# Optimization experiments

Measured on AMD Instinct MI355X. Metric: run time of the kernel, lower is better.

The kernel has to match this reference:

```python
import jax, jax.numpy as jnp
import numpy as np

K_NEIGHBORS = 9  # top_k, dilation=1 for both blocks


def causal_conv1d(x, w, b, dilation):
    # x: [B, Cin, W]; w: [Cout, Cin, K]. Conv1d(padding=p both sides) + Chomp(p) == left-pad only.
    pad = (w.shape[-1] - 1) * dilation
    y = jax.lax.conv_general_dilated(
        x, w, window_strides=(1,), padding=[(pad, 0)], rhs_dilation=(dilation,),
        dimension_numbers=('NCH', 'OIH', 'NCH'))
    return y + b[None, :, None]


def knn_indices(xt, k):
    # xt: [B, N, C] node features. F.normalize(p=2) along channels, then top-k by -||xi-xj||^2.
    xn = xt / jnp.maximum(jnp.linalg.norm(xt, axis=-1, keepdims=True), 1e-12)
    sq = jnp.sum(xn * xn, axis=-1)  # [B, N]
    neg_dist = 2.0 * jnp.einsum('bnc,bmc->bnm', xn, xn) - sq[:, :, None] - sq[:, None, :]
    _, idx = jax.lax.top_k(neg_dist, k)  # [B, N, k]
    return idx


def edge_conv_block(xt, w, b, gamma, beta):
    # xt: [B, N, C]. EdgeConv: max_k gelu(BN(Conv1x1(cat[x_i, x_j - x_i]))) with residual.
    idx = knn_indices(xt, K_NEIGHBORS)
    # gather neighbors: x_j[b,n,k,c] = xt[b, idx[b,n,k], c]
    x_j = jnp.take_along_axis(xt[:, :, None, :], idx[..., None], axis=1)  # [B,N,k,C]
    x_i = xt[:, :, None, :]
    feat = jnp.concatenate([jnp.broadcast_to(x_i, x_j.shape), x_j - x_i], axis=-1)  # [B,N,k,2C]
    h = jnp.einsum('bnkc,oc->bnko', feat, w) + b  # 1x1 conv over 2C -> C
    h = h * gamma + beta  # eval BatchNorm2d (fresh running stats) == affine
    h = jax.nn.gelu(h, approximate=False)
    return xt + jnp.max(h, axis=2)  # residual, [B,N,C]


def ffn_block(xt, w1, b1, g1, be1, w2, b2, g2, be2):
    h = jnp.einsum('bnc,oc->bno', xt, w1) + b1
    h = jax.nn.gelu(h * g1 + be1, approximate=False)
    h = jnp.einsum('bnc,oc->bno', h, w2) + b2
    return h * g2 + be2  # note: this FFN has no residual in the source


def setup_inputs() -> dict:
    key = jax.random.key(0)
    ks = jax.random.split(key, 12)
    B, M, W = 16, 100, 2048
    s = 0.05
    inp = {
        'ts': jax.random.normal(ks[0], (B, M, W), jnp.float32),
        'conv1_w': jax.random.normal(ks[1], (64, M, 3), jnp.float32) * s,
        'conv1_b': jax.random.normal(ks[2], (64,), jnp.float32) * s,
        'conv2_w': jax.random.normal(ks[3], (128, 64, 3), jnp.float32) * s,
        'conv2_b': jax.random.normal(ks[4], (128,), jnp.float32) * s,
        'gconv_w': jax.random.normal(ks[5], (2, 128, 256), jnp.float32) * s,
        'gconv_b': jax.random.normal(ks[6], (2, 128), jnp.float32) * s,
        'gconv_gamma': jnp.ones((2, 128), jnp.float32),
        'gconv_beta': jnp.zeros((2, 128), jnp.float32),
        'ffn1_w': jax.random.normal(ks[7], (2, 128, 128), jnp.float32) * s,
        'ffn1_b': jax.random.normal(ks[8], (2, 128), jnp.float32) * s,
        'ffn1_gamma': jnp.ones((2, 128), jnp.float32),
        'ffn1_beta': jnp.zeros((2, 128), jnp.float32),
        'ffn2_w': jax.random.normal(ks[9], (2, 128, 128), jnp.float32) * s,
        'ffn2_b': jax.random.normal(ks[10], (2, 128), jnp.float32) * s,
        'ffn2_gamma': jnp.ones((2, 128), jnp.float32),
        'ffn2_beta': jnp.zeros((2, 128), jnp.float32),
    }
    return inp


def reference(ts, conv1_w, conv1_b, conv2_w, conv2_b,
              gconv_w, gconv_b, gconv_gamma, gconv_beta,
              ffn1_w, ffn1_b, ffn1_gamma, ffn1_beta,
              ffn2_w, ffn2_b, ffn2_gamma, ffn2_beta):
    # InnerEncoder: two causal dilated Conv1d + ReLU (dropout=0, eval)
    h = jax.nn.relu(causal_conv1d(ts, conv1_w, conv1_b, dilation=1))
    h = jax.nn.relu(causal_conv1d(h, conv2_w, conv2_b, dilation=2))  # [B,128,W]
    xt = h.transpose(0, 2, 1)  # [B, N=W, C=128] nodes
    for blk in range(2):
        xt = edge_conv_block(xt, gconv_w[blk], gconv_b[blk], gconv_gamma[blk], gconv_beta[blk])
        xt = ffn_block(xt, ffn1_w[blk], ffn1_b[blk], ffn1_gamma[blk], ffn1_beta[blk],
                       ffn2_w[blk], ffn2_b[blk], ffn2_gamma[blk], ffn2_beta[blk])
    return xt  # [B, W, 128] == encoderdata.permute(0,2,1)
```

## Files before the change

kernel.cpp:

```cpp
#include <hip/hip_runtime.h>
#include <hip/hip_bf16.h>

#define DEV_INLINE __device__ __forceinline__

typedef short s16x8 __attribute__((ext_vector_type(8)));
typedef float f32x4 __attribute__((ext_vector_type(4)));

DEV_INLINE float gelu_exact(float x) {
    return 0.5f * x * (1.0f + erff(x * 0.70710678118654752440f));
}
DEV_INLINE double gelu64(double x) {
    return 0.5 * x * (1.0 + erf(x * 0.70710678118654752440));
}
DEV_INLINE unsigned short f2bf_rne(float f) {
    unsigned u = __float_as_uint(f);
    unsigned r = u + 0x7FFFu + ((u >> 16) & 1u);
    return (unsigned short)(r >> 16);
}
DEV_INLINE float bf2f(unsigned short h) { return __uint_as_float(((unsigned)h) << 16); }

DEV_INLINE void gload_lds16(const void* g, void* l) {
    __builtin_amdgcn_global_load_lds(
        (const __attribute__((address_space(1))) unsigned int*)g,
        (__attribute__((address_space(3))) unsigned int*)l, 16, 0, 0);
}

DEV_INLINE unsigned med3u32(unsigned a, unsigned b, unsigned c) {
    unsigned d;
    asm("v_med3_u32 %0, %1, %2, %3" : "=v"(d) : "v"(a), "v"(b), "v"(c));
    return d;
}

__global__ __launch_bounds__(256) void conv1_kernel64(
    const float* __restrict__ x, const float* __restrict__ w,
    const float* __restrict__ bias, double* __restrict__ y)
{
    const int b = blockIdx.y;
    const int t0 = blockIdx.x * 32;
    __shared__ double xs[100][34];
    for (int e = threadIdx.x; e < 100 * 34; e += 256) {
        int i = e / 34, u = e - i * 34;
        int t = t0 - 2 + u;
        xs[i][u] = (t >= 0) ? (double)x[(b * 100 + i) * 2048 + t] : 0.0;
    }
    __syncthreads();
    const int o = threadIdx.x & 63;
    const int ts = (threadIdx.x >> 6) * 8;
    double acc[8];
    double bv = (double)bias[o];
#pragma unroll
    for (int j = 0; j < 8; ++j) acc[j] = bv;
    const float* wo = w + o * 300;
    for (int i = 0; i < 100; ++i) {
        double w0 = (double)wo[i * 3 + 0], w1 = (double)wo[i * 3 + 1], w2 = (double)wo[i * 3 + 2];
#pragma unroll
        for (int j = 0; j < 8; ++j) {
            acc[j] = fma(w0, xs[i][ts + j],
                     fma(w1, xs[i][ts + j + 1],
                     fma(w2, xs[i][ts + j + 2], acc[j])));
        }
    }
#pragma unroll
    for (int j = 0; j < 8; ++j)
        y[(b * 64 + o) * 2048 + t0 + ts + j] = fmax(acc[j], 0.0);
}

__global__ __launch_bounds__(256) void conv2_kernel64(
    const double* __restrict__ x, const float* __restrict__ w,
    const float* __restrict__ bias, double* __restrict__ xt)
{
    const int b = blockIdx.y;
    const int t0 = blockIdx.x * 32;
    __shared__ double xs[64][36];
    for (int e = threadIdx.x; e < 64 * 36; e += 256) {
        int i = e / 36, u = e - i * 36;
        int t = t0 - 4 + u;
        xs[i][u] = (t >= 0) ? x[(b * 64 + i) * 2048 + t] : 0.0;
    }
    __syncthreads();
    const int o = threadIdx.x & 127;
    const int ts = (threadIdx.x >> 7) * 16;
    double acc[16];
    double bv = (double)bias[o];
#pragma unroll
    for (int j = 0; j < 16; ++j) acc[j] = bv;
    const float* wo = w + o * 192;
    for (int i = 0; i < 64; ++i) {
        double w0 = (double)wo[i * 3 + 0], w1 = (double)wo[i * 3 + 1], w2 = (double)wo[i * 3 + 2];
#pragma unroll
        for (int j = 0; j < 16; ++j) {
            acc[j] = fma(w0, xs[i][ts + j],
                     fma(w1, xs[i][ts + j + 2],
                     fma(w2, xs[i][ts + j + 4], acc[j])));
        }
    }
#pragma unroll
    for (int j = 0; j < 16; ++j)
        xt[(size_t)(b * 2048 + t0 + ts + j) * 128 + o] = fmax(acc[j], 0.0);
}

__global__ __launch_bounds__(256) void norm_planes_kernel(
    const double* __restrict__ xt64, unsigned short* __restrict__ XH,
    unsigned short* __restrict__ XM, double* __restrict__ XN64,
    double* __restrict__ SQ64)
{
    const int row = blockIdx.x * 4 + (threadIdx.x >> 6);
    const int lane = threadIdx.x & 63;
    double v0 = xt64[(size_t)row * 128 + lane * 2];
    double v1 = xt64[(size_t)row * 128 + lane * 2 + 1];
    double s = v0 * v0 + v1 * v1;
#pragma unroll
    for (int off = 32; off > 0; off >>= 1) s += __shfl_xor(s, off);
    double inv = 1.0 / fmax(sqrt(s), 1e-12);
    double n0 = v0 * inv, n1 = v1 * inv;
    XN64[(size_t)row * 128 + lane * 2]     = n0;
    XN64[(size_t)row * 128 + lane * 2 + 1] = n1;
    double q = n0 * n0 + n1 * n1;
#pragma unroll
    for (int off = 32; off > 0; off >>= 1) q += __shfl_xor(q, off);
    if (lane == 0) SQ64[row] = q;
    float x0 = (float)n0, x1 = (float)n1;
    unsigned short h0 = f2bf_rne(x0), h1 = f2bf_rne(x1);
    unsigned short m0 = f2bf_rne(x0 - bf2f(h0)), m1 = f2bf_rne(x1 - bf2f(h1));
    ushort2 hv; hv.x = h0; hv.y = h1;
    ushort2 mv; mv.x = m0; mv.y = m1;
    *(ushort2*)(XH + (size_t)row * 128 + lane * 2) = hv;
    *(ushort2*)(XM + (size_t)row * 128 + lane * 2) = mv;
}

#define INS9(cc) do { \
    unsigned c_ = (cc); \
    unsigned n0_ = (k0 > c_) ? k0 : c_; \
    unsigned n1_ = med3u32(k0, k1, c_); \
    unsigned n2_ = med3u32(k1, k2, c_); \
    unsigned n3_ = med3u32(k2, k3, c_); \
    unsigned n4_ = med3u32(k3, k4, c_); \
    unsigned n5_ = med3u32(k4, k5, c_); \
    unsigned n6_ = med3u32(k5, k6, c_); \
    unsigned n7_ = med3u32(k6, k7, c_); \
    unsigned n8_ = med3u32(k7, k8, c_); \
    k0 = n0_; k1 = n1_; k2 = n2_; k3 = n3_; k4 = n4_; \
    k5 = n5_; k6 = n6_; k7 = n7_; k8 = n8_; \
} while (0)

__global__ __launch_bounds__(512, 2) void knn_mfma9_kernel(
    const unsigned short* __restrict__ XH, const unsigned short* __restrict__ XM,
    int* __restrict__ cand_out)
{
    __shared__ __align__(16) unsigned char smem[65536];

    const int tid = threadIdx.x, wave = tid >> 6, lane = tid & 63;
    const int bid = blockIdx.x;
    const int j = bid >> 3;
    const int b = (bid & 7) * 2 + (j >> 5);
    const int ntile = (j & 31) >> 1;
    const int mhalf = j & 1;
    const int n0 = ntile * 128;
    const int mstart = mhalf * 1024;
    const unsigned short* Hb = XH + (size_t)b * 2048 * 128;
    const unsigned short* Mb = XM + (size_t)b * 2048 * 128;

    s16x8 aH[4], aM[4];
    {
        int arow = n0 + wave * 16 + (lane & 15);
        const unsigned short* hrow = Hb + (size_t)arow * 128;
        const unsigned short* mrow = Mb + (size_t)arow * 128;
        int cb = (lane >> 4) * 8;
#pragma unroll
        for (int s = 0; s < 4; ++s) {
            aH[s] = *(const s16x8*)(hrow + s * 32 + cb);
            aM[s] = *(const s16x8*)(mrow + s * 32 + cb);
        }
    }

    const unsigned short* Pb = (wave >> 2) ? Mb : Hb;
    const unsigned short* gsrc0; const unsigned short* gsrc1;
    const unsigned short* gsrc2; const unsigned short* gsrc3;
    {
        int r0 = (wave & 3) * 16 + 0 + (lane >> 4), c0 = (lane & 15) ^ (r0 & 7);
        int r1 = (wave & 3) * 16 + 4 + (lane >> 4), c1 = (lane & 15) ^ (r1 & 7);
        int r2 = (wave & 3) * 16 + 8 + (lane >> 4), c2 = (lane & 15) ^ (r2 & 7);
        int r3 = (wave & 3) * 16 + 12 + (lane >> 4), c3 = (lane & 15) ^ (r3 & 7);
        gsrc0 = Pb + (size_t)(mstart + r0) * 128 + c0 * 8;
        gsrc1 = Pb + (size_t)(mstart + r1) * 128 + c1 * 8;
        gsrc2 = Pb + (size_t)(mstart + r2) * 128 + c2 * 8;
        gsrc3 = Pb + (size_t)(mstart + r3) * 128 + c3 * 8;
    }
    const unsigned ldsbase = (wave * 4) * 1024;

    unsigned k0 = 0, k1 = 0, k2 = 0, k3 = 0, k4 = 0, k5 = 0, k6 = 0, k7 = 0, k8 = 0;

    gload_lds16(gsrc0, smem + ldsbase);
    gload_lds16(gsrc1, smem + ldsbase + 1024);
    gload_lds16(gsrc2, smem + ldsbase + 2048);
    gload_lds16(gsrc3, smem + ldsbase + 3072);
    __syncthreads();

    int cur = 0;
    for (int t = 0; t < 16; ++t) {
        if (t < 15) {
            size_t go = (size_t)(t + 1) * 64 * 128;
            unsigned lb = (cur ^ 1) * 32768 + ldsbase;
            gload_lds16(gsrc0 + go, smem + lb);
            gload_lds16(gsrc1 + go, smem + lb + 1024);
            gload_lds16(gsrc2 + go, smem + lb + 2048);
            gload_lds16(gsrc3 + go, smem + lb + 3072);
        }
        const unsigned char* B0 = smem + cur * 32768;
        const unsigned char* B1 = B0 + 16384;
#pragma unroll
        for (int ct = 0; ct < 4; ++ct) {
            f32x4 accA; accA[0] = 0.f; accA[1] = 0.f; accA[2] = 0.f; accA[3] = 0.f;
            f32x4 accB; accB[0] = 0.f; accB[1] = 0.f; accB[2] = 0.f; accB[3] = 0.f;
            int r = ct * 16 + (lane & 15);
#pragma unroll
            for (int s = 0; s < 4; ++s) {
                int off = r * 256 + (((s * 64) + ((lane >> 4) * 16)) ^ ((r & 7) << 4));
                s16x8 bH = *(const s16x8*)(B0 + off);
                s16x8 bM = *(const s16x8*)(B1 + off);
                accA = __builtin_amdgcn_mfma_f32_16x16x32_bf16(bH, aH[s], accA, 0, 0, 0);
                accB = __builtin_amdgcn_mfma_f32_16x16x32_bf16(bM, aH[s], accB, 0, 0, 0);
                accB = __builtin_amdgcn_mfma_f32_16x16x32_bf16(bH, aM[s], accB, 0, 0, 0);
            }
            const unsigned Lb = (unsigned)(255 - (t * 16 + ct * 4));
            unsigned key0 = (__float_as_uint(accA[0] + accB[0] + 2.0f) & 0xFFFFFF00u) | (Lb - 0u);
            unsigned key1 = (__float_as_uint(accA[1] + accB[1] + 2.0f) & 0xFFFFFF00u) | (Lb - 1u);
            unsigned key2 = (__float_as_uint(accA[2] + accB[2] + 2.0f) & 0xFFFFFF00u) | (Lb - 2u);
            unsigned key3 = (__float_as_uint(accA[3] + accB[3] + 2.0f) & 0xFFFFFF00u) | (Lb - 3u);
            INS9(key0);
            INS9(key1);
            INS9(key2);
            INS9(key3);
        }
        __syncthreads();
        cur ^= 1;
    }

    const int g = lane >> 4;
    const int row = b * 2048 + n0 + wave * 16 + (lane & 15);
#pragma unroll
    for (int pass = 0; pass < 16; ++pass) {
        unsigned mykey = k0;
        int L = 255 - (int)(mykey & 0xFFu);
        int mym = mstart + (L >> 4) * 64 + ((L >> 2) & 3) * 16 + g * 4 + (L & 3);
        unsigned bkey = mykey; int bm = mym;
        unsigned ok = (unsigned)__shfl_xor((int)bkey, 16); int om = __shfl_xor(bm, 16);
        bool tk = (ok > bkey) || (ok == bkey && om < bm);
        bkey = tk ? ok : bkey; bm = tk ? om : bm;
        ok = (unsigned)__shfl_xor((int)bkey, 32); om = __shfl_xor(bm, 32);
        tk = (ok > bkey) || (ok == bkey && om < bm);
        bkey = tk ? ok : bkey; bm = tk ? om : bm;
        if (mym == bm) {
            k0 = k1; k1 = k2; k2 = k3; k3 = k4; k4 = k5; k5 = k6; k6 = k7; k7 = k8; k8 = 0;
        }
        if (g == (pass & 3)) cand_out[(size_t)row * 32 + mhalf * 16 + pass] = bm;
    }
}

__global__ __launch_bounds__(256, 4) void rescore5_kernel(
    const double* __restrict__ XN64, const double* __restrict__ SQ64,
    const int* __restrict__ cand, int* __restrict__ idx_out)
{
    const int wid = threadIdx.x >> 6, lane = threadIdx.x & 63;
    const int wb = (blockIdx.x & 7) * 1024 + (blockIdx.x >> 3);
    const int n = wb * 4 + wid;
    const int b = n >> 11;
    const int g = lane >> 4, e = lane & 15;
    const double* Xb = XN64 + (size_t)(b * 2048) * 128;
    const double* SQb = SQ64 + (size_t)b * 2048;

    double2 xq[4];
    const double* xqp = XN64 + (size_t)n * 128;
#pragma unroll
    for (int it = 0; it < 4; ++it)
        xq[it] = *(const double2*)(xqp + it * 32 + e * 2);

    int mi[8];
    double s[8];
#pragma unroll
    for (int bb = 0; bb < 8; ++bb) {
        int m = cand[(size_t)n * 32 + bb * 4 + g];
        mi[bb] = m;
        const double* xm = Xb + (size_t)m * 128;
        double a0 = 0.0, a1 = 0.0;
#pragma unroll
        for (int it = 0; it < 4; ++it) {
            double2 v = *(const double2*)(xm + it * 32 + e * 2);
            a0 = fma(xq[it].x, v.x, a0);
            a1 = fma(xq[it].y, v.y, a1);
        }
        s[bb] = a0 + a1;
    }
#pragma unroll
    for (int bb = 0; bb < 8; ++bb) {
        double d = s[bb];
        d += __shfl_xor(d, 1);
        d += __shfl_xor(d, 2);
        d += __shfl_xor(d, 4);
        d += __shfl_xor(d, 8);
        s[bb] = 2.0 * d - SQb[mi[bb]];
    }
    double mys = s[0]; int mym = mi[0];
#pragma unroll
    for (int q = 1; q < 8; ++q) {
        bool p = (e == q);
        mys = p ? s[q] : mys;
        mym = p ? mi[q] : mym;
    }
    int cnt = 0;
#pragma unroll
    for (int bb = 0; bb < 8; ++bb) {
        cnt += ((s[bb] > mys) || (s[bb] == mys && mi[bb] < mym)) ? 1 : 0;
        double a16 = __shfl_xor(s[bb], 16); int m16 = __shfl_xor(mi[bb], 16);
        cnt += ((a16 > mys) || (a16 == mys && m16 < mym)) ? 1 : 0;
        double a32 = __shfl_xor(s[bb], 32); int m32 = __shfl_xor(mi[bb], 32);
        cnt += ((a32 > mys) || (a32 == mys && m32 < mym)) ? 1 : 0;
        double a48 = __shfl_xor(a16, 32);  int m48 = __shfl_xor(m16, 32);
        cnt += ((a48 > mys) || (a48 == mys && m48 < mym)) ? 1 : 0;
    }
    if (e < 8 && cnt < 9)
        idx_out[(size_t)n * 9 + cnt] = mym;
}

template<int MODE>
__global__ __launch_bounds__(256, 4) void gemm64t_kernel(
    const double* __restrict__ A, const float* __restrict__ W,
    const float* __restrict__ bias, const float* __restrict__ gamma,
    const float* __restrict__ beta, double* __restrict__ out,
    float* __restrict__ out32)
{
    __shared__ double As[64][34];
    __shared__ double Ws[64][34];
    const int bx = (blockIdx.x & 7) * (gridDim.x >> 3) + (blockIdx.x >> 3);
    const int m0 = bx * 64;
    const int j0 = blockIdx.y * 64;
    const int ri = threadIdx.x >> 4, ci = threadIdx.x & 15;
    double acc[4][4];
#pragma unroll
    for (int u = 0; u < 4; ++u)
#pragma unroll
        for (int v = 0; v < 4; ++v) acc[u][v] = 0.0;

    for (int k0 = 0; k0 < 128; k0 += 32) {
        __syncthreads();
        for (int e = threadIdx.x; e < 64 * 16; e += 256) {
            int r = e >> 4, c2 = (e & 15) * 2;
            *(double2*)&As[r][c2] = *(const double2*)(A + (size_t)(m0 + r) * 128 + k0 + c2);
            int jw = j0 + r;
            float2 wv;
            if (MODE == 0) {
                wv = (jw < 128) ? *(const float2*)(W + jw * 256 + k0 + c2)
                                : *(const float2*)(W + (jw - 128) * 256 + 128 + k0 + c2);
            } else {
                wv = *(const float2*)(W + jw * 128 + k0 + c2);
            }
            double2 wd; wd.x = (double)wv.x; wd.y = (double)wv.y;
            *(double2*)&Ws[r][c2] = wd;
        }
        __syncthreads();
        for (int c = 0; c < 32; c += 2) {
            double a0[4], a1[4], w0[4], w1[4];
#pragma unroll
            for (int u = 0; u < 4; ++u) { a0[u] = As[ri + 16 * u][c]; a1[u] = As[ri + 16 * u][c + 1]; }
#pragma unroll
            for (int v = 0; v < 4; ++v) { w0[v] = Ws[ci + 16 * v][c]; w1[v] = Ws[ci + 16 * v][c + 1]; }
#pragma unroll
            for (int u = 0; u < 4; ++u)
#pragma unroll
                for (int v = 0; v < 4; ++v)
                    acc[u][v] = fma(a1[u], w1[v], fma(a0[u], w0[v], acc[u][v]));
        }
    }
#pragma unroll
    for (int u = 0; u < 4; ++u) {
        int row = m0 + ri + 16 * u;
#pragma unroll
        for (int v = 0; v < 4; ++v) {
            int jl = ci + 16 * v;
            double val = acc[u][v];
            if (MODE == 0) {
                out[(size_t)row * 256 + j0 + jl] = val;
            } else {
                int jg = j0 + jl;
                double z = (val + (double)bias[jg]) * (double)gamma[jg] + (double)beta[jg];
                if (MODE == 1) {
                    out[(size_t)row * 128 + jg] = gelu64(z);
                } else {
                    out[(size_t)row * 128 + jg] = z;
                    out32[(size_t)row * 128 + jg] = (float)z;
                }
            }
        }
    }
}

__global__ __launch_bounds__(256) void combine64_kernel(
    double* __restrict__ xt, const double* __restrict__ G,
    const int* __restrict__ idx, const float* __restrict__ bias,
    const float* __restrict__ gamma, const float* __restrict__ beta)
{
    const int wb = (blockIdx.x & 7) * 2048 + (blockIdx.x >> 3);
    const int row = wb * 2 + (threadIdx.x >> 7);
    const int o = threadIdx.x & 127;
    const int b = row >> 11;
    const double* Gb = G + (size_t)(b * 2048) * 256;
    const int* id9 = idx + (size_t)row * 9;
    double g1  = G[(size_t)row * 256 + o];
    double g2i = G[(size_t)row * 256 + 128 + o];
    double base = g1 + (double)bias[o] - g2i;
    double gm = (double)gamma[o], bt = (double)beta[o];
    double mx = -1.0e300;
#pragma unroll
    for (int k = 0; k < 9; ++k) {
        int jn = id9[k];
        double h = base + Gb[(size_t)jn * 256 + 128 + o];
        double z = h * gm + bt;
        mx = fmax(mx, gelu64(z));
    }
    xt[(size_t)row * 128 + o] += mx;
}

template<int MODE>
__global__ __launch_bounds__(256) void gemm128t_kernel(
    const float* __restrict__ A, const float* __restrict__ W,
    const float* __restrict__ bias, const float* __restrict__ gamma,
    const float* __restrict__ beta, float* __restrict__ out)
{
    __shared__ float Al[128][132];
    __shared__ float Wl[128][132];
    const int bx = (blockIdx.x & 7) * (gridDim.x >> 3) + (blockIdx.x >> 3);
    const int m0 = bx * 128;
    const int j0 = blockIdx.y * 128;
    for (int e = threadIdx.x; e < 128 * 32; e += 256) {
        int r = e >> 5, q = e & 31;
        *(float4*)&Al[r][q * 4] = *(const float4*)(A + (size_t)(m0 + r) * 128 + q * 4);
    }
    for (int e = threadIdx.x; e < 128 * 32; e += 256) {
        int jj = e >> 5, q = e & 31;
        int c = q * 4;
        const float* src;
        if (MODE == 0) {
            int jw = j0 + jj;
            src = (jw < 128) ? (W + jw * 256 + c) : (W + (jw - 128) * 256 + 128 + c);
        } else {
            src = W + jj * 128 + c;
        }
        *(float4*)&Wl[jj][c] = *(const float4*)src;
    }
    __syncthreads();
    const int ri = threadIdx.x >> 4, ci = threadIdx.x & 15;
    float acc[8][8];
#pragma unroll
    for (int u = 0; u < 8; ++u)
#pragma unroll
        for (int v = 0; v < 8; ++v) acc[u][v] = 0.0f;
    for (int c = 0; c < 128; c += 4) {
        float4 a4[8];
#pragma unroll
        for (int u = 0; u < 8; ++u) a4[u] = *(const float4*)&Al[ri + 16 * u][c];
#pragma unroll
        for (int v = 0; v < 8; ++v) {
            float4 w4 = *(const float4*)&Wl[ci + 16 * v][c];
#pragma unroll
            for (int u = 0; u < 8; ++u) {
                acc[u][v] = fmaf(a4[u].x, w4.x, fmaf(a4[u].y, w4.y,
                            fmaf(a4[u].z, w4.z, fmaf(a4[u].w, w4.w, acc[u][v]))));
            }
        }
    }
#pragma unroll
    for (int u = 0; u < 8; ++u) {
        int row = m0 + ri + 16 * u;
#pragma unroll
        for (int v = 0; v < 8; ++v) {
            int jn = ci + 16 * v;
            float val = acc[u][v];
            if (MODE == 0) {
                out[(size_t)row * 256 + j0 + jn] = val;
            } else if (MODE == 1) {
                float z = (val + bias[jn]) * gamma[jn] + beta[jn];
                out[(size_t)row * 128 + jn] = gelu_exact(z);
            } else {
                float z = (val + bias[jn]) * gamma[jn] + beta[jn];
                out[(size_t)row * 128 + jn] = z;
            }
        }
    }
}

__global__ __launch_bounds__(256) void combine_kernel(
    const float* __restrict__ xt, const float* __restrict__ G,
    const int* __restrict__ idx, const float* __restrict__ bias,
    const float* __restrict__ gamma, const float* __restrict__ beta,
    float* __restrict__ xt2)
{
    const int wb = (blockIdx.x & 7) * 2048 + (blockIdx.x >> 3);
    const int row = wb * 2 + (threadIdx.x >> 7);
    const int o = threadIdx.x & 127;
    const int b = row >> 11;
    const float* Gb = G + (size_t)(b * 2048) * 256;
    const int* id9 = idx + (size_t)row * 9;
    float g1  = G[(size_t)row * 256 + o];
    float g2i = G[(size_t)row * 256 + 128 + o];
    float base = g1 + bias[o] - g2i;
    float gm = gamma[o], bt = beta[o];
    float mx = -3.4e38f;
#pragma unroll
    for (int k = 0; k < 9; ++k) {
        int jn = id9[k];
        float h = base + Gb[(size_t)jn * 256 + 128 + o];
        float z = h * gm + bt;
        mx = fmaxf(mx, gelu_exact(z));
    }
    xt2[(size_t)row * 128 + o] = xt[(size_t)row * 128 + o] + mx;
}

extern "C" void kernel_launch(void* const* d_in, const int* in_sizes, int n_in,
                              void* d_out, int out_size, void* d_ws, size_t ws_size,
                              hipStream_t stream)
{
    const float* ts       = (const float*)d_in[0];
    const float* conv1_w  = (const float*)d_in[1];
    const float* conv1_b  = (const float*)d_in[2];
    const float* conv2_w  = (const float*)d_in[3];
    const float* conv2_b  = (const float*)d_in[4];
    const float* gconv_w  = (const float*)d_in[5];
    const float* gconv_b  = (const float*)d_in[6];
    const float* gconv_g  = (const float*)d_in[7];
    const float* gconv_be = (const float*)d_in[8];
    const float* ffn1_w   = (const float*)d_in[9];
    const float* ffn1_b   = (const float*)d_in[10];
    const float* ffn1_g   = (const float*)d_in[11];
    const float* ffn1_be  = (const float*)d_in[12];
    const float* ffn2_w   = (const float*)d_in[13];
    const float* ffn2_b   = (const float*)d_in[14];
    const float* ffn2_g   = (const float*)d_in[15];
    const float* ffn2_be  = (const float*)d_in[16];
    (void)in_sizes; (void)n_in; (void)out_size; (void)ws_size;

    char* base = (char*)d_ws;
    double*         XT64   = (double*)(base + 0);
    double*         H1_64  = (double*)(base + 33554432);
    unsigned short* XH     = (unsigned short*)(base + 33554432);
    unsigned short* XM     = (unsigned short*)(base + 41943040);
    int*            CAND   = (int*)   (base + 50331648);
    double*         XN64_1 = (double*)(base + 54525952);
    double*         SQ64_1 = (double*)(base + 88080384);
    double*         G64    = (double*)(base + 33554432);
    double*         H64    = (double*)(base + 33554432);
    float*          XT32P  = (float*) (base + 67108864);
    int*            IDX    = (int*)   (base + 100663296);
    float*          G32    = (float*) (base + 33554432);
    float*          H32    = (float*) (base + 33554432);
    double*         XN64_2 = XT64;
    double*         SQ64_2 = SQ64_1;

    float* fout = (float*)d_out;

    conv1_kernel64<<<dim3(64, 16), 256, 0, stream>>>(ts, conv1_w, conv1_b, H1_64);
    conv2_kernel64<<<dim3(64, 16), 256, 0, stream>>>(H1_64, conv2_w, conv2_b, XT64);

    norm_planes_kernel<<<8192, 256, 0, stream>>>(XT64, XH, XM, XN64_1, SQ64_1);
    knn_mfma9_kernel<<<512, 512, 0, stream>>>(XH, XM, CAND);
    rescore5_kernel<<<8192, 256, 0, stream>>>(XN64_1, SQ64_1, CAND, IDX);
    gemm64t_kernel<0><<<dim3(512, 4), 256, 0, stream>>>(
        XT64, gconv_w, nullptr, nullptr, nullptr, G64, nullptr);
    combine64_kernel<<<16384, 256, 0, stream>>>(
        XT64, G64, IDX, gconv_b, gconv_g, gconv_be);
    gemm64t_kernel<1><<<dim3(512, 2), 256, 0, stream>>>(
        XT64, ffn1_w, ffn1_b, ffn1_g, ffn1_be, H64, nullptr);
    gemm64t_kernel<2><<<dim3(512, 2), 256, 0, stream>>>(
        H64, ffn2_w, ffn2_b, ffn2_g, ffn2_be, XT64, XT32P);

    norm_planes_kernel<<<8192, 256, 0, stream>>>(XT64, XH, XM, XN64_2, SQ64_2);
    knn_mfma9_kernel<<<512, 512, 0, stream>>>(XH, XM, CAND);
    rescore5_kernel<<<8192, 256, 0, stream>>>(XN64_2, SQ64_2, CAND, IDX);
    gemm128t_kernel<0><<<dim3(256, 2), 256, 0, stream>>>(
        XT32P, gconv_w + 32768, nullptr, nullptr, nullptr, G32);
    combine_kernel<<<16384, 256, 0, stream>>>(
        XT32P, G32, IDX, gconv_b + 128, gconv_g + 128, gconv_be + 128, XT32P);
    gemm128t_kernel<1><<<dim3(256, 1), 256, 0, stream>>>(
        XT32P, ffn1_w + 16384, ffn1_b + 128, ffn1_g + 128, ffn1_be + 128, H32);
    gemm128t_kernel<2><<<dim3(256, 1), 256, 0, stream>>>(
        H32, ffn2_w + 16384, ffn2_b + 128, ffn2_g + 128, ffn2_be + 128, fout);
}
```

Baseline: 702.4 us.

## Evaluate GELU only at neighbor min/max and retile fp32 GEMMs with K-chunking

In both combine kernels, the max over nine neighbors of gelu(affine(base+g2)) is replaced by tracking only the min and max of g2 and evaluating GELU at those two points. This relies on GELU composed with an affine map being quasi-convex, so its maximum over an interval lies at an endpoint, and it cuts nine erf evaluations to two. The fp32 GEMM moves from 128x128 tiles with full-K shared memory (about 135KB) to 64-row tiles with 32-wide K chunks and a bounds hint of 4 blocks per SM. This raises occupancy and doubles the grid, at the cost of extra barriers per chunk.

```diff
diff --git a/kernel.cpp b/kernel.cpp
--- a/kernel.cpp
+++ b/kernel.cpp
@@ -409,67 +409,75 @@
     double g2i = G[(size_t)row * 256 + 128 + o];
     double base = g1 + (double)bias[o] - g2i;
     double gm = (double)gamma[o], bt = (double)beta[o];
-    double mx = -1.0e300;
+    double g2mx = -1.0e300, g2mn = 1.0e300;
 #pragma unroll
     for (int k = 0; k < 9; ++k) {
         int jn = id9[k];
-        double h = base + Gb[(size_t)jn * 256 + 128 + o];
-        double z = h * gm + bt;
-        mx = fmax(mx, gelu64(z));
-    }
+        double g2 = Gb[(size_t)jn * 256 + 128 + o];
+        g2mx = fmax(g2mx, g2);
+        g2mn = fmin(g2mn, g2);
+    }
+    double h1 = base + g2mx;
+    double h2 = base + g2mn;
+    double z1 = h1 * gm + bt;
+    double z2 = h2 * gm + bt;
+    double mx = fmax(gelu64(z1), gelu64(z2));
     xt[(size_t)row * 128 + o] += mx;
 }
 
 template<int MODE>
-__global__ __launch_bounds__(256) void gemm128t_kernel(
+__global__ __launch_bounds__(256, 4) void gemm32f_kernel(
     const float* __restrict__ A, const float* __restrict__ W,
     const float* __restrict__ bias, const float* __restrict__ gamma,
     const float* __restrict__ beta, float* __restrict__ out)
 {
-    __shared__ float Al[128][132];
-    __shared__ float Wl[128][132];
+    __shared__ float As[64][36];
+    __shared__ float Ws[128][36];
     const int bx = (blockIdx.x & 7) * (gridDim.x >> 3) + (blockIdx.x >> 3);
-    const int m0 = bx * 128;
+    const int m0 = bx * 64;
     const int j0 = blockIdx.y * 128;
-    for (int e = threadIdx.x; e < 128 * 32; e += 256) {
-        int r = e >> 5, q = e & 31;
-        *(float4*)&Al[r][q * 4] = *(const float4*)(A + (size_t)(m0 + r) * 128 + q * 4);
-    }
-    for (int e = threadIdx.x; e < 128 * 32; e += 256) {
-        int jj = e >> 5, q = e & 31;
-        int c = q * 4;
-        const float* src;
-        if (MODE == 0) {
-            int jw = j0 + jj;
-            src = (jw < 128) ? (W + jw * 256 + c) : (W + (jw - 128) * 256 + 128 + c);
-        } else {
-            src = W + jj * 128 + c;
-        }
-        *(float4*)&Wl[jj][c] = *(const float4*)src;
-    }
-    __syncthreads();
     const int ri = threadIdx.x >> 4, ci = threadIdx.x & 15;
-    float acc[8][8];
-#pragma unroll
-    for (int u = 0; u < 8; ++u)
+    float acc[4][8];
+#pragma unroll
+    for (int u = 0; u < 4; ++u)
 #pragma unroll
         for (int v = 0; v < 8; ++v) acc[u][v] = 0.0f;
-    for (int c = 0; c < 128; c += 4) {
-        float4 a4[8];
-#pragma unroll
-        for (int u = 0; u < 8; ++u) a4[u] = *(const float4*)&Al[ri + 16 * u][c];
-#pragma unroll
-        for (int v = 0; v < 8; ++v) {
-            float4 w4 = *(const float4*)&Wl[ci + 16 * v][c];
-#pragma unroll
-            for (int u = 0; u < 8; ++u) {
-                acc[u][v] = fmaf(a4[u].x, w4.x, fmaf(a4[u].y, w4.y,
-                            fmaf(a4[u].z, w4.z, fmaf(a4[u].w, w4.w, acc[u][v]))));
+
+    for (int k0 = 0; k0 < 128; k0 += 32) {
+        __syncthreads();
+        for (int e = threadIdx.x; e < 64 * 8; e += 256) {
+            int r = e >> 3, q = (e & 7) * 4;
+            *(float4*)&As[r][q] = *(const float4*)(A + (size_t)(m0 + r) * 128 + k0 + q);
+        }
+        for (int e = threadIdx.x; e < 128 * 8; e += 256) {
+            int r = e >> 3, q = (e & 7) * 4;
+            const float* src;
+            if (MODE == 0) {
+                int jw = j0 + r;
+                src = (jw < 128) ? (W + jw * 256 + k0 + q) : (W + (jw - 128) * 256 + 128 + k0 + q);
+            } else {
+                src = W + r * 128 + k0 + q;
             }
-        }
-    }
-#pragma unroll
-    for (int u = 0; u < 8; ++u) {
+            *(float4*)&Ws[r][q] = *(const float4*)src;
+        }
+        __syncthreads();
+        for (int c = 0; c < 32; c += 4) {
+            float4 a4[4];
+#pragma unroll
+            for (int u = 0; u < 4; ++u) a4[u] = *(const float4*)&As[ri + 16 * u][c];
+#pragma unroll
+            for (int v = 0; v < 8; ++v) {
+                float4 w4 = *(const float4*)&Ws[ci + 16 * v][c];
+#pragma unroll
+                for (int u = 0; u < 4; ++u) {
+                    acc[u][v] = fmaf(a4[u].x, w4.x, fmaf(a4[u].y, w4.y,
+                                fmaf(a4[u].z, w4.z, fmaf(a4[u].w, w4.w, acc[u][v]))));
+                }
+            }
+        }
+    }
+#pragma unroll
+    for (int u = 0; u < 4; ++u) {
         int row = m0 + ri + 16 * u;
 #pragma unroll
         for (int v = 0; v < 8; ++v) {
@@ -504,14 +512,17 @@
     float g2i = G[(size_t)row * 256 + 128 + o];
     float base = g1 + bias[o] - g2i;
     float gm = gamma[o], bt = beta[o];
-    float mx = -3.4e38f;
+    float g2mx = -3.4e38f, g2mn = 3.4e38f;
 #pragma unroll
     for (int k = 0; k < 9; ++k) {
         int jn = id9[k];
-        float h = base + Gb[(size_t)jn * 256 + 128 + o];
-        float z = h * gm + bt;
-        mx = fmaxf(mx, gelu_exact(z));
-    }
+        float g2 = Gb[(size_t)jn * 256 + 128 + o];
+        g2mx = fmaxf(g2mx, g2);
+        g2mn = fminf(g2mn, g2);
+    }
+    float z1 = (base + g2mx) * gm + bt;
+    float z2 = (base + g2mn) * gm + bt;
+    float mx = fmaxf(gelu_exact(z1), gelu_exact(z2));
     xt2[(size_t)row * 128 + o] = xt[(size_t)row * 128 + o] + mx;
 }
 
@@ -575,12 +586,12 @@
     norm_planes_kernel<<<8192, 256, 0, stream>>>(XT64, XH, XM, XN64_2, SQ64_2);
     knn_mfma9_kernel<<<512, 512, 0, stream>>>(XH, XM, CAND);
     rescore5_kernel<<<8192, 256, 0, stream>>>(XN64_2, SQ64_2, CAND, IDX);
-    gemm128t_kernel<0><<<dim3(256, 2), 256, 0, stream>>>(
+    gemm32f_kernel<0><<<dim3(512, 2), 256, 0, stream>>>(
         XT32P, gconv_w + 32768, nullptr, nullptr, nullptr, G32);
     combine_kernel<<<16384, 256, 0, stream>>>(
         XT32P, G32, IDX, gconv_b + 128, gconv_g + 128, gconv_be + 128, XT32P);
-    gemm128t_kernel<1><<<dim3(256, 1), 256, 0, stream>>>(
+    gemm32f_kernel<1><<<dim3(512, 1), 256, 0, stream>>>(
         XT32P, ffn1_w + 16384, ffn1_b + 128, ffn1_g + 128, ffn1_be + 128, H32);
-    gemm128t_kernel<2><<<dim3(256, 1), 256, 0, stream>>>(
+    gemm32f_kernel<2><<<dim3(512, 1), 256, 0, stream>>>(
         H32, ffn2_w + 16384, ffn2_b + 128, ffn2_g + 128, ffn2_be + 128, fout);
 }
```

Result: faster. 633.9 us (-9.7%).
